# Performance work log

Measured on AMD Instinct MI355X. Metric: run time of the kernel, lower is better.

The kernel has to match this reference:

```python
import jax, jax.numpy as jnp
import numpy as np

H = 1024   # hidden_size
V = 32000  # output_size (vocab)
B = 64     # batch
S = 2048   # encoder seq_len


def setup_inputs() -> dict:
    key = jax.random.key(0)
    ks = jax.random.split(key, 12)
    sc = 0.02
    return {
        "input_seq": jax.random.randint(ks[0], (B,), 0, V),
        "last_hidden": jax.random.normal(ks[1], (1, B, H), jnp.float32),
        "encoder_outputs": jax.random.normal(ks[2], (S, B, H), jnp.float32),
        "emb": jax.random.normal(ks[3], (V, H), jnp.float32) * sc,
        "w_ih": jax.random.normal(ks[4], (3 * H, H), jnp.float32) * sc,
        "w_hh": jax.random.normal(ks[5], (3 * H, H), jnp.float32) * sc,
        "b_ih": jnp.zeros((3 * H,), jnp.float32),
        "b_hh": jnp.zeros((3 * H,), jnp.float32),
        "attn_w": jax.random.normal(ks[6], (H, H), jnp.float32) * sc,
        "attn_b": jnp.zeros((H,), jnp.float32),
        "concat_w": jax.random.normal(ks[7], (H, 2 * H), jnp.float32) * sc,
        "concat_b": jnp.zeros((H,), jnp.float32),
        "out_w": jax.random.normal(ks[8], (V, H), jnp.float32) * sc,
        "out_b": jnp.zeros((V,), jnp.float32),
    }


def _forward(input_seq, last_hidden, encoder_outputs, emb, w_ih, w_hh, b_ih, b_hh,
             attn_w, attn_b, concat_w, concat_b, out_w, out_b):
    # 1. embedding (dropout = identity in eval)
    x = emb[input_seq]                      # [b, h]
    h = last_hidden[0]                      # [b, h]
    # 2. single-step GRU (PyTorch gate order: reset, update, new)
    gx = x @ w_ih.T + b_ih                  # [b, 3h]
    gh = h @ w_hh.T + b_hh                  # [b, 3h]
    r = jax.nn.sigmoid(gx[:, :H] + gh[:, :H])
    z = jax.nn.sigmoid(gx[:, H:2 * H] + gh[:, H:2 * H])
    n = jnp.tanh(gx[:, 2 * H:] + r * gh[:, 2 * H:])
    h_new = (1.0 - z) * n + z * h           # [b, h] = rnn_output
    # 3. Luong 'general' attention: score = y . (W enc + b)
    proj = jnp.einsum('sbh,gh->sbg', encoder_outputs, attn_w) + attn_b  # [s,b,h]
    scores = jnp.einsum('bh,sbh->bs', h_new, proj)                      # [b,s]
    attn_weights = jax.nn.softmax(scores, axis=-1)                      # [b,s]
    # 4. context = weights bmm encoder_outputs
    context = jnp.einsum('bs,sbh->bh', attn_weights, encoder_outputs)   # [b,h]
    # 5. concat -> linear -> tanh -> out
    cat = jnp.concatenate([h_new, context], axis=-1)                    # [b,2h]
    concat_output = jnp.tanh(cat @ concat_w.T + concat_b)               # [b,h]
    output = concat_output @ out_w.T + out_b                            # [b,V]
    return output, h_new[None], attn_weights[:, None, :]


def reference(input_seq, last_hidden, encoder_outputs, emb, w_ih, w_hh, b_ih, b_hh,
              attn_w, attn_b, concat_w, concat_b, out_w, out_b):
    return _forward(input_seq, last_hidden, encoder_outputs, emb, w_ih, w_hh, b_ih,
                    b_hh, attn_w, attn_b, concat_w, concat_b, out_w, out_b)
```

## Files before the change

### kernel.cpp

```cpp
#include <hip/hip_runtime.h>

#define HS 1024
#define VS 32000
#define BS 64
#define SS 2048
#define NCH 64
#define SCH (SS/NCH)

typedef __attribute__((ext_vector_type(4))) float f4v;
typedef __attribute__((ext_vector_type(8))) short s8v;

__device__ __forceinline__ float sigmf(float x) { return 1.0f / (1.0f + __expf(-x)); }

__device__ __forceinline__ short bf16c(float f) {
  unsigned u = __builtin_bit_cast(unsigned, f);
  u = (u + 0x7FFFu + ((u >> 16) & 1u)) >> 16;
  return (short)u;
}

__global__ __launch_bounds__(256) void k_prep(const int* __restrict__ idx,
    const float* __restrict__ emb, const float* __restrict__ hid,
    const float* __restrict__ aw, float* __restrict__ ht,
    short* __restrict__ fx, short* __restrict__ fh, short* __restrict__ awf) {
  int t = blockIdx.x * 256 + threadIdx.x;
  {
    int lane = t & 63, nt = (t >> 6) & 63, kt = t >> 12;
    int kr = kt * 32 + ((lane >> 4) & 3) * 8;
    int col = nt * 16 + (lane & 15);
    const float* sp = aw + (size_t)kr * HS + col;
    s8v v;
#pragma unroll
    for (int j = 0; j < 8; j++) v[j] = bf16c(sp[(size_t)j * HS]);
    *(s8v*)(awf + (size_t)t * 8) = v;
  }
  if (t < 65536) {
    int b = t >> 10, k = t & 1023;
    ht[k * BS + b] = hid[(size_t)b * HS + k];
  }
  if (t < 8192) {
    int lane = t & 63, ct = (t >> 6) & 3, kt = t >> 8;
    int col = ct * 16 + (lane & 15);
    int kr = kt * 32 + ((lane >> 4) & 3) * 8;
    const float* sp = emb + (size_t)idx[col] * HS + kr;
    s8v v;
#pragma unroll
    for (int j = 0; j < 8; j++) v[j] = bf16c(sp[j]);
    *(s8v*)(fx + (size_t)t * 8) = v;
  } else if (t < 16384) {
    int t2 = t - 8192;
    int lane = t2 & 63, ct = (t2 >> 6) & 3, kt = t2 >> 8;
    int col = ct * 16 + (lane & 15);
    int kr = kt * 32 + ((lane >> 4) & 3) * 8;
    const float* sp = hid + (size_t)col * HS + kr;
    s8v v;
#pragma unroll
    for (int j = 0; j < 8; j++) v[j] = bf16c(sp[j]);
    *(s8v*)(fh + (size_t)t2 * 8) = v;
  }
}

template<int K, int OL>
__global__ __launch_bounds__(256) void mfsk(
    const float* __restrict__ W0, const short* __restrict__ xf0,
    const float* __restrict__ bias0, void* __restrict__ dst0,
    const float* __restrict__ W1, const short* __restrict__ xf1,
    const float* __restrict__ bias1, void* __restrict__ dst1) {
  const float* W    = blockIdx.y ? W1 : W0;
  const short* xf   = blockIdx.y ? xf1 : xf0;
  const float* bias = blockIdx.y ? bias1 : bias0;
  void* dst         = blockIdx.y ? dst1 : dst0;
  int lane = threadIdx.x & 63;
  int ks = threadIdx.x >> 6;
  int mt = blockIdx.x;
  int row = mt * 16 + (lane & 15);
  const int KW = (K / 32) / 4;
  const float* wp = W + (size_t)row * K + ((lane >> 4) * 8);
  const s8v* xp = (const s8v*)xf + lane;
  f4v acc0 = {0,0,0,0}, acc1 = {0,0,0,0}, acc2 = {0,0,0,0}, acc3 = {0,0,0,0};
#pragma unroll 4
  for (int kk = 0; kk < KW; kk++) {
    int kt = ks * KW + kk;
    float4 wa = *(const float4*)(wp + (size_t)kt * 32);
    float4 wb = *(const float4*)(wp + (size_t)kt * 32 + 4);
    s8v a;
    a[0] = bf16c(wa.x); a[1] = bf16c(wa.y); a[2] = bf16c(wa.z); a[3] = bf16c(wa.w);
    a[4] = bf16c(wb.x); a[5] = bf16c(wb.y); a[6] = bf16c(wb.z); a[7] = bf16c(wb.w);
    const s8v* xk = xp + (size_t)kt * 256;
    acc0 = __builtin_amdgcn_mfma_f32_16x16x32_bf16(a, xk[0],   acc0, 0, 0, 0);
    acc1 = __builtin_amdgcn_mfma_f32_16x16x32_bf16(a, xk[64],  acc1, 0, 0, 0);
    acc2 = __builtin_amdgcn_mfma_f32_16x16x32_bf16(a, xk[128], acc2, 0, 0, 0);
    acc3 = __builtin_amdgcn_mfma_f32_16x16x32_bf16(a, xk[192], acc3, 0, 0, 0);
  }
  __shared__ float red[4][4][4][64];
#pragma unroll
  for (int r = 0; r < 4; r++) {
    red[ks][0][r][lane] = acc0[r];
    red[ks][1][r][lane] = acc1[r];
    red[ks][2][r][lane] = acc2[r];
    red[ks][3][r][lane] = acc3[r];
  }
  __syncthreads();
  int ct = ks;
  int rr0 = mt * 16 + (lane >> 4) * 4;
  int col = ct * 16 + (lane & 15);
#pragma unroll
  for (int r = 0; r < 4; r++) {
    float v = red[0][ct][r][lane] + red[1][ct][r][lane] +
              red[2][ct][r][lane] + red[3][ct][r][lane] + bias[rr0 + r];
    if (OL == 0)
      ((float*)dst)[(size_t)(rr0 + r) * BS + col] = v;
    else
      ((short*)dst)[(size_t)col * HS + rr0 + r] = bf16c(tanhf(v));
  }
}

__global__ __launch_bounds__(256) void k_hnew(const float* __restrict__ gxt,
    const float* __restrict__ ght, const float* __restrict__ ht,
    float* __restrict__ out_h, short* __restrict__ fcat) {
  int tid = blockIdx.x * 256 + threadIdx.x;
  int b = tid & 63, i = tid >> 6;
  float r = sigmf(gxt[i * BS + b] + ght[i * BS + b]);
  float z = sigmf(gxt[(HS + i) * BS + b] + ght[(HS + i) * BS + b]);
  float n = tanhf(gxt[(2 * HS + i) * BS + b] + r * ght[(2 * HS + i) * BS + b]);
  float hn = (1.0f - z) * n + z * ht[i * BS + b];
  out_h[(size_t)b * HS + i] = hn;
  int kt = i >> 5, j = i & 7;
  int lane = (b & 15) | (((i >> 3) & 3) << 4);
  int ct = b >> 4;
  fcat[((size_t)((kt * 4 + ct) * 64 + lane)) * 8 + j] = bf16c(hn);
}

__global__ __launch_bounds__(256) void k_qgemm(const float* __restrict__ hnr,
    const short* __restrict__ awf, float* __restrict__ qrow) {
  int lane = threadIdx.x & 63;
  int mt = threadIdx.x >> 6;
  int nt = blockIdx.x;
  const float* ap = hnr + (size_t)(mt * 16 + (lane & 15)) * HS + ((lane >> 4) * 8);
  const s8v* bp = (const s8v*)awf + (size_t)nt * 64 + lane;
  f4v acc = {0,0,0,0};
#pragma unroll 4
  for (int kt = 0; kt < 32; kt++) {
    float4 wa = *(const float4*)(ap + kt * 32);
    float4 wb = *(const float4*)(ap + kt * 32 + 4);
    s8v a;
    a[0] = bf16c(wa.x); a[1] = bf16c(wa.y); a[2] = bf16c(wa.z); a[3] = bf16c(wa.w);
    a[4] = bf16c(wb.x); a[5] = bf16c(wb.y); a[6] = bf16c(wb.z); a[7] = bf16c(wb.w);
    acc = __builtin_amdgcn_mfma_f32_16x16x32_bf16(a, bp[(size_t)kt * 4096], acc, 0, 0, 0);
  }
  int r0 = mt * 16 + (lane >> 4) * 4;
  int hcol = nt * 16 + (lane & 15);
#pragma unroll
  for (int r = 0; r < 4; r++)
    qrow[(size_t)(r0 + r) * HS + hcol] = acc[r];
}

__global__ __launch_bounds__(256, 4) void k_attn(const float* __restrict__ enc,
    const float* __restrict__ qrow, float* __restrict__ scores,
    float* __restrict__ mch, float* __restrict__ lch, float* __restrict__ ctxp) {
  int lane = threadIdx.x & 63;
  int w = blockIdx.x * 4 + (threadIdx.x >> 6);
  int b = w & 63;
  int ch = w >> 6;
  const float* qb = qrow + (size_t)b * HS + lane * 4;
  float4 q0 = *(const float4*)(qb + 0);
  float4 q1 = *(const float4*)(qb + 256);
  float4 q2 = *(const float4*)(qb + 512);
  float4 q3 = *(const float4*)(qb + 768);
  int s0 = ch * SCH;
  const float* ep = enc + ((size_t)s0 * BS + b) * HS + lane * 4;
  float4 e0 = *(const float4*)(ep + 0);
  float4 e1 = *(const float4*)(ep + 256);
  float4 e2 = *(const float4*)(ep + 512);
  float4 e3 = *(const float4*)(ep + 768);
  float m = -1e30f, l = 0.f;
  float4 a0 = {0,0,0,0}, a1 = {0,0,0,0}, a2 = {0,0,0,0}, a3 = {0,0,0,0};
  for (int si = 0; si < SCH; si++) {
    float4 c0 = e0, c1 = e1, c2 = e2, c3 = e3;
    if (si + 1 < SCH) {
      const float* np = ep + (size_t)BS * HS;
      e0 = *(const float4*)(np + 0);
      e1 = *(const float4*)(np + 256);
      e2 = *(const float4*)(np + 512);
      e3 = *(const float4*)(np + 768);
    }
    ep += (size_t)BS * HS;
    float d0 = fmaf(c0.x,q0.x, fmaf(c0.y,q0.y, fmaf(c0.z,q0.z, c0.w*q0.w)));
    float d1 = fmaf(c1.x,q1.x, fmaf(c1.y,q1.y, fmaf(c1.z,q1.z, c1.w*q1.w)));
    float d2 = fmaf(c2.x,q2.x, fmaf(c2.y,q2.y, fmaf(c2.z,q2.z, c2.w*q2.w)));
    float d3 = fmaf(c3.x,q3.x, fmaf(c3.y,q3.y, fmaf(c3.z,q3.z, c3.w*q3.w)));
    float p = (d0 + d1) + (d2 + d3);
#pragma unroll
    for (int off = 32; off; off >>= 1) p += __shfl_xor(p, off, 64);
    if (lane == 0) scores[(size_t)b * SS + s0 + si] = p;
    float mn = fmaxf(m, p);
    float sc = __expf(m - mn);
    float pr = __expf(p - mn);
    l = fmaf(l, sc, pr);
    a0.x = fmaf(a0.x, sc, pr * c0.x); a0.y = fmaf(a0.y, sc, pr * c0.y);
    a0.z = fmaf(a0.z, sc, pr * c0.z); a0.w = fmaf(a0.w, sc, pr * c0.w);
    a1.x = fmaf(a1.x, sc, pr * c1.x); a1.y = fmaf(a1.y, sc, pr * c1.y);
    a1.z = fmaf(a1.z, sc, pr * c1.z); a1.w = fmaf(a1.w, sc, pr * c1.w);
    a2.x = fmaf(a2.x, sc, pr * c2.x); a2.y = fmaf(a2.y, sc, pr * c2.y);
    a2.z = fmaf(a2.z, sc, pr * c2.z); a2.w = fmaf(a2.w, sc, pr * c2.w);
    a3.x = fmaf(a3.x, sc, pr * c3.x); a3.y = fmaf(a3.y, sc, pr * c3.y);
    a3.z = fmaf(a3.z, sc, pr * c3.z); a3.w = fmaf(a3.w, sc, pr * c3.w);
    m = mn;
  }
  if (lane == 0) { mch[b * NCH + ch] = m; lch[b * NCH + ch] = l; }
  float* cp = ctxp + ((size_t)(b * NCH + ch)) * HS + lane * 4;
  *(float4*)(cp + 0)   = a0;
  *(float4*)(cp + 256) = a1;
  *(float4*)(cp + 512) = a2;
  *(float4*)(cp + 768) = a3;
}

__global__ __launch_bounds__(256) void k_combine(const float* __restrict__ mch,
    const float* __restrict__ lch, const float* __restrict__ ctxp,
    const float* __restrict__ scores, short* __restrict__ fcat,
    float* __restrict__ wout) {
  int b = blockIdx.x;
  int t = threadIdx.x;
  __shared__ float sm[NCH], sl[NCH], ssc[NCH];
  if (t < NCH) { sm[t] = mch[b * NCH + t]; sl[t] = lch[b * NCH + t]; }
  __syncthreads();
  float mstar = -1e30f;
  for (int c = 0; c < NCH; c++) mstar = fmaxf(mstar, sm[c]);
  if (t < NCH) ssc[t] = __expf(sm[t] - mstar);
  __syncthreads();
  float L = 0.f;
  for (int c = 0; c < NCH; c++) L = fmaf(sl[c], ssc[c], L);
  float invL = 1.0f / L;
  int h = blockIdx.y * 256 + t;
  float acc = 0.f;
  for (int c = 0; c < NCH; c++)
    acc = fmaf(ctxp[((size_t)(b * NCH + c)) * HS + h], ssc[c], acc);
  float ctx = acc * invL;
  int kc = HS + h;
  int kt = kc >> 5, j = kc & 7;
  int lane2 = (b & 15) | (((kc >> 3) & 3) << 4);
  int ct = b >> 4;
  fcat[((size_t)((kt * 4 + ct) * 64 + lane2)) * 8 + j] = bf16c(ctx);
  if (blockIdx.y == 0)
    for (int s = t; s < SS; s += 256)
      wout[(size_t)b * SS + s] = __expf(scores[(size_t)b * SS + s] - mstar) * invL;
}

__global__ __launch_bounds__(256) void k_out2(const short* __restrict__ cbf,
    const float* __restrict__ ow, const float* __restrict__ ob,
    float* __restrict__ out0) {
  int lane = threadIdx.x & 63;
  int wv = threadIdx.x >> 6;
  int nt = blockIdx.x * 4 + wv;
  int v0 = nt * 16;
  const float* wp = ow + (size_t)(v0 + (lane & 15)) * HS + ((lane >> 4) * 8);
  const short* a0p = cbf + (size_t)(0  + (lane & 15)) * HS + ((lane >> 4) * 8);
  const short* a1p = a0p + (size_t)16 * HS;
  const short* a2p = a0p + (size_t)32 * HS;
  const short* a3p = a0p + (size_t)48 * HS;
  f4v acc0 = {0,0,0,0}, acc1 = {0,0,0,0}, acc2 = {0,0,0,0}, acc3 = {0,0,0,0};
#pragma unroll 4
  for (int kt = 0; kt < 32; kt++) {
    float4 wa = *(const float4*)(wp + kt * 32);
    float4 wb = *(const float4*)(wp + kt * 32 + 4);
    s8v bf;
    bf[0] = bf16c(wa.x); bf[1] = bf16c(wa.y); bf[2] = bf16c(wa.z); bf[3] = bf16c(wa.w);
    bf[4] = bf16c(wb.x); bf[5] = bf16c(wb.y); bf[6] = bf16c(wb.z); bf[7] = bf16c(wb.w);
    s8v fa0 = *(const s8v*)(a0p + kt * 32);
    s8v fa1 = *(const s8v*)(a1p + kt * 32);
    s8v fa2 = *(const s8v*)(a2p + kt * 32);
    s8v fa3 = *(const s8v*)(a3p + kt * 32);
    acc0 = __builtin_amdgcn_mfma_f32_16x16x32_bf16(fa0, bf, acc0, 0, 0, 0);
    acc1 = __builtin_amdgcn_mfma_f32_16x16x32_bf16(fa1, bf, acc1, 0, 0, 0);
    acc2 = __builtin_amdgcn_mfma_f32_16x16x32_bf16(fa2, bf, acc2, 0, 0, 0);
    acc3 = __builtin_amdgcn_mfma_f32_16x16x32_bf16(fa3, bf, acc3, 0, 0, 0);
  }
  float bv = ob[v0 + (lane & 15)];
  int rb = (lane >> 4) * 4;
  int vc = v0 + (lane & 15);
#pragma unroll
  for (int r = 0; r < 4; r++) {
    out0[(size_t)(0  + rb + r) * VS + vc] = acc0[r] + bv;
    out0[(size_t)(16 + rb + r) * VS + vc] = acc1[r] + bv;
    out0[(size_t)(32 + rb + r) * VS + vc] = acc2[r] + bv;
    out0[(size_t)(48 + rb + r) * VS + vc] = acc3[r] + bv;
  }
}

extern "C" void kernel_launch(void* const* d_in, const int* in_sizes, int n_in,
                              void* d_out, int out_size, void* d_ws, size_t ws_size,
                              hipStream_t stream) {
  const int*   idx  = (const int*)d_in[0];
  const float* hid  = (const float*)d_in[1];
  const float* enc  = (const float*)d_in[2];
  const float* emb  = (const float*)d_in[3];
  const float* w_ih = (const float*)d_in[4];
  const float* w_hh = (const float*)d_in[5];
  const float* b_ih = (const float*)d_in[6];
  const float* b_hh = (const float*)d_in[7];
  const float* aw   = (const float*)d_in[8];
  const float* cw   = (const float*)d_in[10];
  const float* cb   = (const float*)d_in[11];
  const float* ow   = (const float*)d_in[12];
  const float* ob   = (const float*)d_in[13];

  float* out0  = (float*)d_out;
  float* out_h = out0 + (size_t)BS * VS;
  float* out_w = out_h + (size_t)BS * HS;

  float* ws   = (float*)d_ws;
  float* gxt  = ws;
  float* ght  = gxt + (size_t)3 * HS * BS;
  float* ht   = ght + (size_t)3 * HS * BS;
  float* qrow = ht  + (size_t)HS * BS;
  float* scr  = qrow + (size_t)HS * BS;
  float* mch  = scr + (size_t)BS * SS;
  float* lch  = mch + (size_t)BS * NCH;
  float* ctxp = lch + (size_t)BS * NCH;
  short* awf  = (short*)(ctxp + (size_t)BS * NCH * HS);
  short* fx   = awf + (size_t)HS * HS;
  short* fh   = fx  + (size_t)HS * BS;
  short* fcat = fh  + (size_t)HS * BS;
  short* cbf  = fcat + (size_t)2 * HS * BS;

  k_prep   <<<dim3(512), dim3(256), 0, stream>>>(idx, emb, hid, aw, ht, fx, fh, awf);
  mfsk<HS, 0><<<dim3(3 * HS / 16, 2), dim3(256), 0, stream>>>(
      w_ih, fx, b_ih, gxt, w_hh, fh, b_hh, ght);
  k_hnew   <<<dim3(HS * BS / 256), dim3(256), 0, stream>>>(gxt, ght, ht, out_h, fcat);
  k_qgemm  <<<dim3(HS / 16), dim3(256), 0, stream>>>(out_h, awf, qrow);
  k_attn   <<<dim3(BS * NCH / 4), dim3(256), 0, stream>>>(enc, qrow, scr, mch, lch, ctxp);
  k_combine<<<dim3(BS, 4), dim3(256), 0, stream>>>(mch, lch, ctxp, scr, fcat, out_w);
  mfsk<2 * HS, 1><<<dim3(HS / 16, 1), dim3(256), 0, stream>>>(
      cw, fcat, cb, cbf, cw, fcat, cb, cbf);
  k_out2   <<<dim3(VS / 64), dim3(256), 0, stream>>>(cbf, ow, ob, out0);
}
```

Measured before the change: 210.5 us.

## Merge pre- and post-attention kernels into persistent kernels with grid barriers

Fuses the prep, GRU GEMMs, hidden update and query GEMM into one persistent kernel, and the softmax combine, concat GEMM and vocab projection into another. Stages are separated by atomic-counter grid barriers instead of kernel launches. This is meant to remove launch and drain overheads between small dependent stages. It relies on all blocks being co-resident, adds a memset, and risks deadlock or spin overhead if occupancy assumptions fail.

```diff
diff --git a/kernel.cpp b/kernel.cpp
--- a/kernel.cpp
+++ b/kernel.cpp
@@ -18,140 +18,152 @@
   return (short)u;
 }
 
-__global__ __launch_bounds__(256) void k_prep(const int* __restrict__ idx,
-    const float* __restrict__ emb, const float* __restrict__ hid,
-    const float* __restrict__ aw, float* __restrict__ ht,
-    short* __restrict__ fx, short* __restrict__ fh, short* __restrict__ awf) {
-  int t = blockIdx.x * 256 + threadIdx.x;
+__device__ __forceinline__ void gridbar(unsigned* cnt, unsigned target) {
+  __syncthreads();
+  __threadfence();
+  if (threadIdx.x == 0) {
+    __hip_atomic_fetch_add(cnt, 1u, __ATOMIC_ACQ_REL, __HIP_MEMORY_SCOPE_AGENT);
+    while (__hip_atomic_load(cnt, __ATOMIC_ACQUIRE, __HIP_MEMORY_SCOPE_AGENT) < target)
+      __builtin_amdgcn_s_sleep(2);
+  }
+  __syncthreads();
+  __threadfence();
+}
+
+__global__ __launch_bounds__(256, 2) void k_front(
+    const int* __restrict__ idx, const float* __restrict__ emb,
+    const float* __restrict__ hid, const float* __restrict__ aw,
+    const float* __restrict__ w_ih, const float* __restrict__ w_hh,
+    const float* __restrict__ b_ih, const float* __restrict__ b_hh,
+    float* __restrict__ ht, short* __restrict__ fx, short* __restrict__ fh,
+    short* __restrict__ awf, float* __restrict__ gxt, float* __restrict__ ght,
+    float* __restrict__ out_h, short* __restrict__ fcat,
+    float* __restrict__ qrow, unsigned* __restrict__ bar) {
+  __shared__ float red[4][4][4][64];
+  const int bid = blockIdx.x, tid = threadIdx.x;
+  const int gid = bid * 256 + tid;
+
+  for (int t = gid; t < 131072; t += 98304) {
+    {
+      int lane = t & 63, nt = (t >> 6) & 63, kt = t >> 12;
+      int kr = kt * 32 + ((lane >> 4) & 3) * 8;
+      int col = nt * 16 + (lane & 15);
+      const float* sp = aw + (size_t)kr * HS + col;
+      s8v v;
+#pragma unroll
+      for (int j = 0; j < 8; j++) v[j] = bf16c(sp[(size_t)j * HS]);
+      *(s8v*)(awf + (size_t)t * 8) = v;
+    }
+    if (t < 65536) {
+      int b = t >> 10, k = t & 1023;
+      ht[k * BS + b] = hid[(size_t)b * HS + k];
+    }
+    if (t < 8192) {
+      int lane = t & 63, ct = (t >> 6) & 3, kt = t >> 8;
+      int col = ct * 16 + (lane & 15);
+      int kr = kt * 32 + ((lane >> 4) & 3) * 8;
+      const float* sp = emb + (size_t)idx[col] * HS + kr;
+      s8v v;
+#pragma unroll
+      for (int j = 0; j < 8; j++) v[j] = bf16c(sp[j]);
+      *(s8v*)(fx + (size_t)t * 8) = v;
+    } else if (t < 16384) {
+      int t2 = t - 8192;
+      int lane = t2 & 63, ct = (t2 >> 6) & 3, kt = t2 >> 8;
+      int col = ct * 16 + (lane & 15);
+      int kr = kt * 32 + ((lane >> 4) & 3) * 8;
+      const float* sp = hid + (size_t)col * HS + kr;
+      s8v v;
+#pragma unroll
+      for (int j = 0; j < 8; j++) v[j] = bf16c(sp[j]);
+      *(s8v*)(fh + (size_t)t2 * 8) = v;
+    }
+  }
+  gridbar(bar, 384);
+
   {
-    int lane = t & 63, nt = (t >> 6) & 63, kt = t >> 12;
-    int kr = kt * 32 + ((lane >> 4) & 3) * 8;
-    int col = nt * 16 + (lane & 15);
-    const float* sp = aw + (size_t)kr * HS + col;
-    s8v v;
-#pragma unroll
-    for (int j = 0; j < 8; j++) v[j] = bf16c(sp[(size_t)j * HS]);
-    *(s8v*)(awf + (size_t)t * 8) = v;
-  }
-  if (t < 65536) {
-    int b = t >> 10, k = t & 1023;
-    ht[k * BS + b] = hid[(size_t)b * HS + k];
-  }
-  if (t < 8192) {
-    int lane = t & 63, ct = (t >> 6) & 3, kt = t >> 8;
+    int y = (bid >= 192) ? 1 : 0;
+    int mt = bid - y * 192;
+    const float* W    = y ? w_hh : w_ih;
+    const short* xf   = y ? fh : fx;
+    const float* bias = y ? b_hh : b_ih;
+    float* dst        = y ? ght : gxt;
+    int lane = tid & 63;
+    int ks = tid >> 6;
+    int row = mt * 16 + (lane & 15);
+    const float* wp = W + (size_t)row * HS + ((lane >> 4) * 8);
+    const s8v* xp = (const s8v*)xf + lane;
+    f4v acc0 = {0,0,0,0}, acc1 = {0,0,0,0}, acc2 = {0,0,0,0}, acc3 = {0,0,0,0};
+#pragma unroll 4
+    for (int kk = 0; kk < 8; kk++) {
+      int kt = ks * 8 + kk;
+      float4 wa = *(const float4*)(wp + (size_t)kt * 32);
+      float4 wb = *(const float4*)(wp + (size_t)kt * 32 + 4);
+      s8v a;
+      a[0] = bf16c(wa.x); a[1] = bf16c(wa.y); a[2] = bf16c(wa.z); a[3] = bf16c(wa.w);
+      a[4] = bf16c(wb.x); a[5] = bf16c(wb.y); a[6] = bf16c(wb.z); a[7] = bf16c(wb.w);
+      const s8v* xk = xp + (size_t)kt * 256;
+      acc0 = __builtin_amdgcn_mfma_f32_16x16x32_bf16(a, xk[0],   acc0, 0, 0, 0);
+      acc1 = __builtin_amdgcn_mfma_f32_16x16x32_bf16(a, xk[64],  acc1, 0, 0, 0);
+      acc2 = __builtin_amdgcn_mfma_f32_16x16x32_bf16(a, xk[128], acc2, 0, 0, 0);
+      acc3 = __builtin_amdgcn_mfma_f32_16x16x32_bf16(a, xk[192], acc3, 0, 0, 0);
+    }
+#pragma unroll
+    for (int r = 0; r < 4; r++) {
+      red[ks][0][r][lane] = acc0[r];
+      red[ks][1][r][lane] = acc1[r];
+      red[ks][2][r][lane] = acc2[r];
+      red[ks][3][r][lane] = acc3[r];
+    }
+    __syncthreads();
+    int ct = ks;
+    int rr0 = mt * 16 + (lane >> 4) * 4;
     int col = ct * 16 + (lane & 15);
-    int kr = kt * 32 + ((lane >> 4) & 3) * 8;
-    const float* sp = emb + (size_t)idx[col] * HS + kr;
-    s8v v;
-#pragma unroll
-    for (int j = 0; j < 8; j++) v[j] = bf16c(sp[j]);
-    *(s8v*)(fx + (size_t)t * 8) = v;
-  } else if (t < 16384) {
-    int t2 = t - 8192;
-    int lane = t2 & 63, ct = (t2 >> 6) & 3, kt = t2 >> 8;
-    int col = ct * 16 + (lane & 15);
-    int kr = kt * 32 + ((lane >> 4) & 3) * 8;
-    const float* sp = hid + (size_t)col * HS + kr;
-    s8v v;
-#pragma unroll
-    for (int j = 0; j < 8; j++) v[j] = bf16c(sp[j]);
-    *(s8v*)(fh + (size_t)t2 * 8) = v;
-  }
-}
-
-template<int K, int OL>
-__global__ __launch_bounds__(256) void mfsk(
-    const float* __restrict__ W0, const short* __restrict__ xf0,
-    const float* __restrict__ bias0, void* __restrict__ dst0,
-    const float* __restrict__ W1, const short* __restrict__ xf1,
-    const float* __restrict__ bias1, void* __restrict__ dst1) {
-  const float* W    = blockIdx.y ? W1 : W0;
-  const short* xf   = blockIdx.y ? xf1 : xf0;
-  const float* bias = blockIdx.y ? bias1 : bias0;
-  void* dst         = blockIdx.y ? dst1 : dst0;
-  int lane = threadIdx.x & 63;
-  int ks = threadIdx.x >> 6;
-  int mt = blockIdx.x;
-  int row = mt * 16 + (lane & 15);
-  const int KW = (K / 32) / 4;
-  const float* wp = W + (size_t)row * K + ((lane >> 4) * 8);
-  const s8v* xp = (const s8v*)xf + lane;
-  f4v acc0 = {0,0,0,0}, acc1 = {0,0,0,0}, acc2 = {0,0,0,0}, acc3 = {0,0,0,0};
+#pragma unroll
+    for (int r = 0; r < 4; r++) {
+      float v = red[0][ct][r][lane] + red[1][ct][r][lane] +
+                red[2][ct][r][lane] + red[3][ct][r][lane] + bias[rr0 + r];
+      dst[(size_t)(rr0 + r) * BS + col] = v;
+    }
+  }
+  gridbar(bar, 768);
+
+  if (gid < 65536) {
+    int b = gid & 63, i = gid >> 6;
+    float r = sigmf(gxt[i * BS + b] + ght[i * BS + b]);
+    float z = sigmf(gxt[(HS + i) * BS + b] + ght[(HS + i) * BS + b]);
+    float n = tanhf(gxt[(2 * HS + i) * BS + b] + r * ght[(2 * HS + i) * BS + b]);
+    float hn = (1.0f - z) * n + z * ht[i * BS + b];
+    out_h[(size_t)b * HS + i] = hn;
+    int kt = i >> 5, j = i & 7;
+    int lane = (b & 15) | (((i >> 3) & 3) << 4);
+    int ct = b >> 4;
+    fcat[((size_t)((kt * 4 + ct) * 64 + lane)) * 8 + j] = bf16c(hn);
+  }
+  gridbar(bar, 1152);
+
+  if (bid < 64) {
+    int lane = tid & 63;
+    int mt = tid >> 6;
+    int nt = bid;
+    const float* ap = out_h + (size_t)(mt * 16 + (lane & 15)) * HS + ((lane >> 4) * 8);
+    const s8v* bp = (const s8v*)awf + (size_t)nt * 64 + lane;
+    f4v acc = {0,0,0,0};
 #pragma unroll 4
-  for (int kk = 0; kk < KW; kk++) {
-    int kt = ks * KW + kk;
-    float4 wa = *(const float4*)(wp + (size_t)kt * 32);
-    float4 wb = *(const float4*)(wp + (size_t)kt * 32 + 4);
-    s8v a;
-    a[0] = bf16c(wa.x); a[1] = bf16c(wa.y); a[2] = bf16c(wa.z); a[3] = bf16c(wa.w);
-    a[4] = bf16c(wb.x); a[5] = bf16c(wb.y); a[6] = bf16c(wb.z); a[7] = bf16c(wb.w);
-    const s8v* xk = xp + (size_t)kt * 256;
-    acc0 = __builtin_amdgcn_mfma_f32_16x16x32_bf16(a, xk[0],   acc0, 0, 0, 0);
-    acc1 = __builtin_amdgcn_mfma_f32_16x16x32_bf16(a, xk[64],  acc1, 0, 0, 0);
-    acc2 = __builtin_amdgcn_mfma_f32_16x16x32_bf16(a, xk[128], acc2, 0, 0, 0);
-    acc3 = __builtin_amdgcn_mfma_f32_16x16x32_bf16(a, xk[192], acc3, 0, 0, 0);
-  }
-  __shared__ float red[4][4][4][64];
-#pragma unroll
-  for (int r = 0; r < 4; r++) {
-    red[ks][0][r][lane] = acc0[r];
-    red[ks][1][r][lane] = acc1[r];
-    red[ks][2][r][lane] = acc2[r];
-    red[ks][3][r][lane] = acc3[r];
-  }
-  __syncthreads();
-  int ct = ks;
-  int rr0 = mt * 16 + (lane >> 4) * 4;
-  int col = ct * 16 + (lane & 15);
-#pragma unroll
-  for (int r = 0; r < 4; r++) {
-    float v = red[0][ct][r][lane] + red[1][ct][r][lane] +
-              red[2][ct][r][lane] + red[3][ct][r][lane] + bias[rr0 + r];
-    if (OL == 0)
-      ((float*)dst)[(size_t)(rr0 + r) * BS + col] = v;
-    else
-      ((short*)dst)[(size_t)col * HS + rr0 + r] = bf16c(tanhf(v));
-  }
-}
-
-__global__ __launch_bounds__(256) void k_hnew(const float* __restrict__ gxt,
-    const float* __restrict__ ght, const float* __restrict__ ht,
-    float* __restrict__ out_h, short* __restrict__ fcat) {
-  int tid = blockIdx.x * 256 + threadIdx.x;
-  int b = tid & 63, i = tid >> 6;
-  float r = sigmf(gxt[i * BS + b] + ght[i * BS + b]);
-  float z = sigmf(gxt[(HS + i) * BS + b] + ght[(HS + i) * BS + b]);
-  float n = tanhf(gxt[(2 * HS + i) * BS + b] + r * ght[(2 * HS + i) * BS + b]);
-  float hn = (1.0f - z) * n + z * ht[i * BS + b];
-  out_h[(size_t)b * HS + i] = hn;
-  int kt = i >> 5, j = i & 7;
-  int lane = (b & 15) | (((i >> 3) & 3) << 4);
-  int ct = b >> 4;
-  fcat[((size_t)((kt * 4 + ct) * 64 + lane)) * 8 + j] = bf16c(hn);
-}
-
-__global__ __launch_bounds__(256) void k_qgemm(const float* __restrict__ hnr,
-    const short* __restrict__ awf, float* __restrict__ qrow) {
-  int lane = threadIdx.x & 63;
-  int mt = threadIdx.x >> 6;
-  int nt = blockIdx.x;
-  const float* ap = hnr + (size_t)(mt * 16 + (lane & 15)) * HS + ((lane >> 4) * 8);
-  const s8v* bp = (const s8v*)awf + (size_t)nt * 64 + lane;
-  f4v acc = {0,0,0,0};
-#pragma unroll 4
-  for (int kt = 0; kt < 32; kt++) {
-    float4 wa = *(const float4*)(ap + kt * 32);
-    float4 wb = *(const float4*)(ap + kt * 32 + 4);
-    s8v a;
-    a[0] = bf16c(wa.x); a[1] = bf16c(wa.y); a[2] = bf16c(wa.z); a[3] = bf16c(wa.w);
-    a[4] = bf16c(wb.x); a[5] = bf16c(wb.y); a[6] = bf16c(wb.z); a[7] = bf16c(wb.w);
-    acc = __builtin_amdgcn_mfma_f32_16x16x32_bf16(a, bp[(size_t)kt * 4096], acc, 0, 0, 0);
-  }
-  int r0 = mt * 16 + (lane >> 4) * 4;
-  int hcol = nt * 16 + (lane & 15);
-#pragma unroll
-  for (int r = 0; r < 4; r++)
-    qrow[(size_t)(r0 + r) * HS + hcol] = acc[r];
+    for (int kt = 0; kt < 32; kt++) {
+      float4 wa = *(const float4*)(ap + kt * 32);
+      float4 wb = *(const float4*)(ap + kt * 32 + 4);
+      s8v a;
+      a[0] = bf16c(wa.x); a[1] = bf16c(wa.y); a[2] = bf16c(wa.z); a[3] = bf16c(wa.w);
+      a[4] = bf16c(wb.x); a[5] = bf16c(wb.y); a[6] = bf16c(wb.z); a[7] = bf16c(wb.w);
+      acc = __builtin_amdgcn_mfma_f32_16x16x32_bf16(a, bp[(size_t)kt * 4096], acc, 0, 0, 0);
+    }
+    int r0 = mt * 16 + (lane >> 4) * 4;
+    int hcol = nt * 16 + (lane & 15);
+#pragma unroll
+    for (int r = 0; r < 4; r++)
+      qrow[(size_t)(r0 + r) * HS + hcol] = acc[r];
+  }
 }
 
 __global__ __launch_bounds__(256, 4) void k_attn(const float* __restrict__ enc,
@@ -214,75 +226,125 @@
   *(float4*)(cp + 768) = a3;
 }
 
-__global__ __launch_bounds__(256) void k_combine(const float* __restrict__ mch,
-    const float* __restrict__ lch, const float* __restrict__ ctxp,
-    const float* __restrict__ scores, short* __restrict__ fcat,
-    float* __restrict__ wout) {
-  int b = blockIdx.x;
-  int t = threadIdx.x;
+__global__ __launch_bounds__(256, 2) void k_back(
+    const float* __restrict__ mch, const float* __restrict__ lch,
+    const float* __restrict__ ctxp, const float* __restrict__ scores,
+    short* __restrict__ fcat, float* __restrict__ wout,
+    const float* __restrict__ cw, const float* __restrict__ cb,
+    short* __restrict__ cbf, const float* __restrict__ ow,
+    const float* __restrict__ ob, float* __restrict__ out0,
+    unsigned* __restrict__ bar) {
   __shared__ float sm[NCH], sl[NCH], ssc[NCH];
-  if (t < NCH) { sm[t] = mch[b * NCH + t]; sl[t] = lch[b * NCH + t]; }
-  __syncthreads();
-  float mstar = -1e30f;
-  for (int c = 0; c < NCH; c++) mstar = fmaxf(mstar, sm[c]);
-  if (t < NCH) ssc[t] = __expf(sm[t] - mstar);
-  __syncthreads();
-  float L = 0.f;
-  for (int c = 0; c < NCH; c++) L = fmaf(sl[c], ssc[c], L);
-  float invL = 1.0f / L;
-  int h = blockIdx.y * 256 + t;
-  float acc = 0.f;
-  for (int c = 0; c < NCH; c++)
-    acc = fmaf(ctxp[((size_t)(b * NCH + c)) * HS + h], ssc[c], acc);
-  float ctx = acc * invL;
-  int kc = HS + h;
-  int kt = kc >> 5, j = kc & 7;
-  int lane2 = (b & 15) | (((kc >> 3) & 3) << 4);
-  int ct = b >> 4;
-  fcat[((size_t)((kt * 4 + ct) * 64 + lane2)) * 8 + j] = bf16c(ctx);
-  if (blockIdx.y == 0)
-    for (int s = t; s < SS; s += 256)
-      wout[(size_t)b * SS + s] = __expf(scores[(size_t)b * SS + s] - mstar) * invL;
-}
-
-__global__ __launch_bounds__(256) void k_out2(const short* __restrict__ cbf,
-    const float* __restrict__ ow, const float* __restrict__ ob,
-    float* __restrict__ out0) {
-  int lane = threadIdx.x & 63;
-  int wv = threadIdx.x >> 6;
-  int nt = blockIdx.x * 4 + wv;
-  int v0 = nt * 16;
-  const float* wp = ow + (size_t)(v0 + (lane & 15)) * HS + ((lane >> 4) * 8);
-  const short* a0p = cbf + (size_t)(0  + (lane & 15)) * HS + ((lane >> 4) * 8);
-  const short* a1p = a0p + (size_t)16 * HS;
-  const short* a2p = a0p + (size_t)32 * HS;
-  const short* a3p = a0p + (size_t)48 * HS;
-  f4v acc0 = {0,0,0,0}, acc1 = {0,0,0,0}, acc2 = {0,0,0,0}, acc3 = {0,0,0,0};
+  __shared__ float red[4][4][4][64];
+  const int bid = blockIdx.x, tid = threadIdx.x;
+
+  if (bid < 256) {
+    int b = bid & 63, by = bid >> 6;
+    int t = tid;
+    if (t < NCH) { sm[t] = mch[b * NCH + t]; sl[t] = lch[b * NCH + t]; }
+    __syncthreads();
+    float mstar = -1e30f;
+    for (int c = 0; c < NCH; c++) mstar = fmaxf(mstar, sm[c]);
+    if (t < NCH) ssc[t] = __expf(sm[t] - mstar);
+    __syncthreads();
+    float L = 0.f;
+    for (int c = 0; c < NCH; c++) L = fmaf(sl[c], ssc[c], L);
+    float invL = 1.0f / L;
+    int h = by * 256 + t;
+    float acc = 0.f;
+    for (int c = 0; c < NCH; c++)
+      acc = fmaf(ctxp[((size_t)(b * NCH + c)) * HS + h], ssc[c], acc);
+    float ctx = acc * invL;
+    int kc = HS + h;
+    int kt = kc >> 5, j = kc & 7;
+    int lane2 = (b & 15) | (((kc >> 3) & 3) << 4);
+    int ct = b >> 4;
+    fcat[((size_t)((kt * 4 + ct) * 64 + lane2)) * 8 + j] = bf16c(ctx);
+    if (by == 0)
+      for (int s = t; s < SS; s += 256)
+        wout[(size_t)b * SS + s] = __expf(scores[(size_t)b * SS + s] - mstar) * invL;
+  }
+  gridbar(bar, 500);
+
+  if (bid < 64) {
+    int lane = tid & 63;
+    int ks = tid >> 6;
+    int mt = bid;
+    int row = mt * 16 + (lane & 15);
+    const float* wp = cw + (size_t)row * (2 * HS) + ((lane >> 4) * 8);
+    const s8v* xp = (const s8v*)fcat + lane;
+    f4v acc0 = {0,0,0,0}, acc1 = {0,0,0,0}, acc2 = {0,0,0,0}, acc3 = {0,0,0,0};
 #pragma unroll 4
-  for (int kt = 0; kt < 32; kt++) {
-    float4 wa = *(const float4*)(wp + kt * 32);
-    float4 wb = *(const float4*)(wp + kt * 32 + 4);
-    s8v bf;
-    bf[0] = bf16c(wa.x); bf[1] = bf16c(wa.y); bf[2] = bf16c(wa.z); bf[3] = bf16c(wa.w);
-    bf[4] = bf16c(wb.x); bf[5] = bf16c(wb.y); bf[6] = bf16c(wb.z); bf[7] = bf16c(wb.w);
-    s8v fa0 = *(const s8v*)(a0p + kt * 32);
-    s8v fa1 = *(const s8v*)(a1p + kt * 32);
-    s8v fa2 = *(const s8v*)(a2p + kt * 32);
-    s8v fa3 = *(const s8v*)(a3p + kt * 32);
-    acc0 = __builtin_amdgcn_mfma_f32_16x16x32_bf16(fa0, bf, acc0, 0, 0, 0);
-    acc1 = __builtin_amdgcn_mfma_f32_16x16x32_bf16(fa1, bf, acc1, 0, 0, 0);
-    acc2 = __builtin_amdgcn_mfma_f32_16x16x32_bf16(fa2, bf, acc2, 0, 0, 0);
-    acc3 = __builtin_amdgcn_mfma_f32_16x16x32_bf16(fa3, bf, acc3, 0, 0, 0);
-  }
-  float bv = ob[v0 + (lane & 15)];
-  int rb = (lane >> 4) * 4;
-  int vc = v0 + (lane & 15);
-#pragma unroll
-  for (int r = 0; r < 4; r++) {
-    out0[(size_t)(0  + rb + r) * VS + vc] = acc0[r] + bv;
-    out0[(size_t)(16 + rb + r) * VS + vc] = acc1[r] + bv;
-    out0[(size_t)(32 + rb + r) * VS + vc] = acc2[r] + bv;
-    out0[(size_t)(48 + rb + r) * VS + vc] = acc3[r] + bv;
+    for (int kk = 0; kk < 16; kk++) {
+      int kt = ks * 16 + kk;
+      float4 wa = *(const float4*)(wp + (size_t)kt * 32);
+      float4 wb = *(const float4*)(wp + (size_t)kt * 32 + 4);
+      s8v a;
+      a[0] = bf16c(wa.x); a[1] = bf16c(wa.y); a[2] = bf16c(wa.z); a[3] = bf16c(wa.w);
+      a[4] = bf16c(wb.x); a[5] = bf16c(wb.y); a[6] = bf16c(wb.z); a[7] = bf16c(wb.w);
+      const s8v* xk = xp + (size_t)kt * 256;
+      acc0 = __builtin_amdgcn_mfma_f32_16x16x32_bf16(a, xk[0],   acc0, 0, 0, 0);
+      acc1 = __builtin_amdgcn_mfma_f32_16x16x32_bf16(a, xk[64],  acc1, 0, 0, 0);
+      acc2 = __builtin_amdgcn_mfma_f32_16x16x32_bf16(a, xk[128], acc2, 0, 0, 0);
+      acc3 = __builtin_amdgcn_mfma_f32_16x16x32_bf16(a, xk[192], acc3, 0, 0, 0);
+    }
+#pragma unroll
+    for (int r = 0; r < 4; r++) {
+      red[ks][0][r][lane] = acc0[r];
+      red[ks][1][r][lane] = acc1[r];
+      red[ks][2][r][lane] = acc2[r];
+      red[ks][3][r][lane] = acc3[r];
+    }
+    __syncthreads();
+    int ct = ks;
+    int rr0 = mt * 16 + (lane >> 4) * 4;
+    int col = ct * 16 + (lane & 15);
+#pragma unroll
+    for (int r = 0; r < 4; r++) {
+      float v = red[0][ct][r][lane] + red[1][ct][r][lane] +
+                red[2][ct][r][lane] + red[3][ct][r][lane] + cb[rr0 + r];
+      cbf[(size_t)col * HS + rr0 + r] = bf16c(tanhf(v));
+    }
+  }
+  gridbar(bar, 1000);
+
+  {
+    int lane = tid & 63;
+    int wv = tid >> 6;
+    int nt = bid * 4 + wv;
+    int v0 = nt * 16;
+    const float* wp = ow + (size_t)(v0 + (lane & 15)) * HS + ((lane >> 4) * 8);
+    const short* a0p = cbf + (size_t)(0  + (lane & 15)) * HS + ((lane >> 4) * 8);
+    const short* a1p = a0p + (size_t)16 * HS;
+    const short* a2p = a0p + (size_t)32 * HS;
+    const short* a3p = a0p + (size_t)48 * HS;
+    f4v acc0 = {0,0,0,0}, acc1 = {0,0,0,0}, acc2 = {0,0,0,0}, acc3 = {0,0,0,0};
+#pragma unroll 4
+    for (int kt = 0; kt < 32; kt++) {
+      float4 wa = *(const float4*)(wp + kt * 32);
+      float4 wb = *(const float4*)(wp + kt * 32 + 4);
+      s8v bf;
+      bf[0] = bf16c(wa.x); bf[1] = bf16c(wa.y); bf[2] = bf16c(wa.z); bf[3] = bf16c(wa.w);
+      bf[4] = bf16c(wb.x); bf[5] = bf16c(wb.y); bf[6] = bf16c(wb.z); bf[7] = bf16c(wb.w);
+      s8v fa0 = *(const s8v*)(a0p + kt * 32);
+      s8v fa1 = *(const s8v*)(a1p + kt * 32);
+      s8v fa2 = *(const s8v*)(a2p + kt * 32);
+      s8v fa3 = *(const s8v*)(a3p + kt * 32);
+      acc0 = __builtin_amdgcn_mfma_f32_16x16x32_bf16(fa0, bf, acc0, 0, 0, 0);
+      acc1 = __builtin_amdgcn_mfma_f32_16x16x32_bf16(fa1, bf, acc1, 0, 0, 0);
+      acc2 = __builtin_amdgcn_mfma_f32_16x16x32_bf16(fa2, bf, acc2, 0, 0, 0);
+      acc3 = __builtin_amdgcn_mfma_f32_16x16x32_bf16(fa3, bf, acc3, 0, 0, 0);
+    }
+    float bv = ob[v0 + (lane & 15)];
+    int rb = (lane >> 4) * 4;
+    int vc = v0 + (lane & 15);
+#pragma unroll
+    for (int r = 0; r < 4; r++) {
+      out0[(size_t)(0  + rb + r) * VS + vc] = acc0[r] + bv;
+      out0[(size_t)(16 + rb + r) * VS + vc] = acc1[r] + bv;
+      out0[(size_t)(32 + rb + r) * VS + vc] = acc2[r] + bv;
+      out0[(size_t)(48 + rb + r) * VS + vc] = acc3[r] + bv;
+    }
   }
 }
 
@@ -321,15 +383,15 @@
   short* fh   = fx  + (size_t)HS * BS;
   short* fcat = fh  + (size_t)HS * BS;
   short* cbf  = fcat + (size_t)2 * HS * BS;
-
-  k_prep   <<<dim3(512), dim3(256), 0, stream>>>(idx, emb, hid, aw, ht, fx, fh, awf);
-  mfsk<HS, 0><<<dim3(3 * HS / 16, 2), dim3(256), 0, stream>>>(
-      w_ih, fx, b_ih, gxt, w_hh, fh, b_hh, ght);
-  k_hnew   <<<dim3(HS * BS / 256), dim3(256), 0, stream>>>(gxt, ght, ht, out_h, fcat);
-  k_qgemm  <<<dim3(HS / 16), dim3(256), 0, stream>>>(out_h, awf, qrow);
-  k_attn   <<<dim3(BS * NCH / 4), dim3(256), 0, stream>>>(enc, qrow, scr, mch, lch, ctxp);
-  k_combine<<<dim3(BS, 4), dim3(256), 0, stream>>>(mch, lch, ctxp, scr, fcat, out_w);
-  mfsk<2 * HS, 1><<<dim3(HS / 16, 1), dim3(256), 0, stream>>>(
-      cw, fcat, cb, cbf, cw, fcat, cb, cbf);
-  k_out2   <<<dim3(VS / 64), dim3(256), 0, stream>>>(cbf, ow, ob, out0);
-}
+  unsigned* barf = (unsigned*)((((uintptr_t)(cbf + (size_t)HS * BS)) + 255)
+                               & ~(uintptr_t)255);
+  unsigned* barb = barf + 64;
+
+  hipMemsetAsync(barf, 0, 512, stream);
+  k_front<<<dim3(384), dim3(256), 0, stream>>>(
+      idx, emb, hid, aw, w_ih, w_hh, b_ih, b_hh,
+      ht, fx, fh, awf, gxt, ght, out_h, fcat, qrow, barf);
+  k_attn <<<dim3(BS * NCH / 4), dim3(256), 0, stream>>>(enc, qrow, scr, mch, lch, ctxp);
+  k_back <<<dim3(VS / 64), dim3(256), 0, stream>>>(
+      mch, lch, ctxp, scr, fcat, out_w, cw, cb, cbf, ow, ob, out0, barb);
+}
```

Measured after the change: 812.8 us. 3.86x slower.
